# Kernel optimization log

Hardware: AMD Instinct MI355X
Metric: run time of the kernel (lower is better)

## Reference

```python
import jax, jax.numpy as jnp
import numpy as np

B, N, C, H = 4, 2048, 384, 6
D = C // H                       # head_dim = 64
HID = 4 * C                      # mlp hidden = 1536
SCALE = D ** -0.5
EPS = 1e-5                       # torch nn.LayerNorm default


def setup_inputs() -> dict:
    key = jax.random.key(0)
    ks = jax.random.split(key, 8)
    s = 0.02
    return {
        "x": jax.random.normal(ks[0], (B, N, C), jnp.float32),
        "ln1_g": jnp.ones((C,), jnp.float32),
        "ln1_b": jnp.zeros((C,), jnp.float32),
        "w_qkv": jax.random.normal(ks[1], (3 * C, C), jnp.float32) * s,
        "w_proj": jax.random.normal(ks[2], (C, C), jnp.float32) * s,
        "b_proj": jnp.zeros((C,), jnp.float32),
        "ln2_g": jnp.ones((C,), jnp.float32),
        "ln2_b": jnp.zeros((C,), jnp.float32),
        "w_fc1": jax.random.normal(ks[3], (HID, C), jnp.float32) * s,
        "b_fc1": jnp.zeros((HID,), jnp.float32),
        "w_fc2": jax.random.normal(ks[4], (C, HID), jnp.float32) * s,
        "b_fc2": jnp.zeros((C,), jnp.float32),
    }


def _layernorm(x, g, b):
    mu = jnp.mean(x, axis=-1, keepdims=True)
    var = jnp.mean(jnp.square(x - mu), axis=-1, keepdims=True)
    return (x - mu) * jax.lax.rsqrt(var + EPS) * g + b


def _bf16_round(x):
    # emulate the .bfloat16() cast after each residual (precision truncation)
    return x.astype(jnp.bfloat16).astype(jnp.float32)


def reference(x, ln1_g, ln1_b, w_qkv, w_proj, b_proj,
              ln2_g, ln2_b, w_fc1, b_fc1, w_fc2, b_fc2):
    # ---- attention branch (quant=False => HMQ ops are pass-through) ----
    h = _layernorm(x, ln1_g, ln1_b)                       # [B,N,C]
    qkv = jnp.einsum('bnc,oc->bno', h, w_qkv)             # [B,N,3C]
    qkv = qkv.reshape(B, N, 3, H, D).transpose(2, 0, 3, 1, 4)  # [3,B,H,N,D]
    q, k, v = qkv[0], qkv[1], qkv[2]
    attn = jnp.einsum('bhnd,bhmd->bhnm', q, k) * SCALE    # [B,H,N,N]
    attn = jax.nn.softmax(attn, axis=-1)
    o = jnp.einsum('bhnm,bhmd->bhnd', attn, v)            # [B,H,N,D]
    o = o.transpose(0, 2, 1, 3).reshape(B, N, C)
    o = jnp.einsum('bnc,oc->bno', o, w_proj) + b_proj
    x = _bf16_round(x + o)

    # ---- MLP branch ----
    h = _layernorm(x, ln2_g, ln2_b)
    h = jnp.einsum('bnc,hc->bnh', h, w_fc1) + b_fc1       # [B,N,HID]
    h = jax.nn.gelu(h, approximate=False)
    h = jnp.einsum('bnh,ch->bnc', h, w_fc2) + b_fc2       # [B,N,C]
    x = _bf16_round(x + h)
    return x
```

## Files before the change

### kernel.cpp

```cpp
#include <hip/hip_runtime.h>
#include <cstdint>
#include <cstddef>

#define DI __device__ __forceinline__

typedef __attribute__((ext_vector_type(8))) short short8;
typedef __attribute__((ext_vector_type(4))) float f32x4;
typedef unsigned int u32;
typedef unsigned short u16;

DI u16 rne_bf16(float f) {
  union { float f; u32 u; } v; v.f = f;
  u32 b = v.u;
  return (u16)((b + 0x7fffu + ((b >> 16) & 1u)) >> 16);
}
DI float bf2f(u16 h) {
  union { u32 u; float f; } v; v.u = ((u32)h) << 16;
  return v.f;
}

DI void gl2lds16(const void* g, void* l) {
  __builtin_amdgcn_global_load_lds(
      (const __attribute__((address_space(1))) u32*)g,
      (__attribute__((address_space(3))) u32*)l, 16, 0, 0);
}

DI void bar() {
  asm volatile("" ::: "memory");
  __builtin_amdgcn_s_barrier();
  asm volatile("" ::: "memory");
}

template<int ROWS>
DI void stage_swz(const u16* src, int ld, char* ldsb, int tid) {
  int wbase = tid & ~63;
  #pragma unroll
  for (int c = 0; c < (ROWS * 8) / 256; ++c) {
    int g = c * 256 + tid;
    int row = g >> 3;
    int sgr = (g & 7) ^ (row & 7);
    gl2lds16(src + row * ld + sgr * 8, ldsb + (size_t)(c * 256 + wbase) * 16);
  }
}

DI short8 lds_frag(const char* base, int row, int k0) {
  return *(const short8*)(base + row * 128 + ((k0 * 2) ^ ((row & 7) << 4)));
}

DI f32x4 mfma16(short8 a, short8 b, f32x4 c) {
  return __builtin_amdgcn_mfma_f32_16x16x32_bf16(a, b, c, 0, 0, 0);
}

__global__ __launch_bounds__(256) void cvt_w(
    const float* __restrict__ a, const float* __restrict__ b,
    const float* __restrict__ c, const float* __restrict__ d,
    u16* __restrict__ oa, u16* __restrict__ ob, u16* __restrict__ oc,
    u16* __restrict__ od) {
  int i = blockIdx.x * 256 + threadIdx.x;
  if (i < 442368) oa[i] = rne_bf16(a[i]);
  else if (i < 589824) ob[i - 442368] = rne_bf16(b[i - 442368]);
  else if (i < 1179648) oc[i - 589824] = rne_bf16(c[i - 589824]);
  else if (i < 1769472) od[i - 1179648] = rne_bf16(d[i - 1179648]);
}

template<int INBF>
__global__ __launch_bounds__(256) void ln_k(
    const void* __restrict__ xin, const float* __restrict__ gam,
    const float* __restrict__ bet, u16* __restrict__ out) {
  int row = blockIdx.x * 4 + (threadIdx.x >> 6);
  int lane = threadIdx.x & 63;
  float v[6];
  if (INBF) {
    const u16* x = (const u16*)xin + (size_t)row * 384 + lane * 6;
    #pragma unroll
    for (int j = 0; j < 6; ++j) v[j] = bf2f(x[j]);
  } else {
    const float* x = (const float*)xin + (size_t)row * 384 + lane * 6;
    #pragma unroll
    for (int j = 0; j < 6; ++j) v[j] = x[j];
  }
  float s = 0.f;
  #pragma unroll
  for (int j = 0; j < 6; ++j) s += v[j];
  #pragma unroll
  for (int d = 1; d < 64; d <<= 1) s += __shfl_xor(s, d);
  float mu = s * (1.f / 384.f);
  float q = 0.f;
  #pragma unroll
  for (int j = 0; j < 6; ++j) { float t = v[j] - mu; q += t * t; }
  #pragma unroll
  for (int d = 1; d < 64; d <<= 1) q += __shfl_xor(q, d);
  float rstd = rsqrtf(q * (1.f / 384.f) + 1e-5f);
  #pragma unroll
  for (int j = 0; j < 6; ++j) {
    int c = lane * 6 + j;
    out[(size_t)row * 384 + c] = rne_bf16((v[j] - mu) * rstd * gam[c] + bet[c]);
  }
}

struct EpiP {
  const float* bias;
  const float* residf;
  const u16* residb;
  u16* outb;
  float* outf;
  u16* q; u16* k; u16* v;
};

template<int EPI, int MT>
__global__ __launch_bounds__(256) void gemm_bt(
    const u16* __restrict__ A, const u16* __restrict__ W, int K, EpiP p) {
  constexpr int ABUF = MT * 128;
  constexpr int NC = (MT == 128) ? 4 : 2;
  __shared__ char lds[2 * (ABUF + 16384)];
  int tid = threadIdx.x, lane = tid & 63, wid = tid >> 6;
  int wr = (MT == 128) ? (wid >> 1) * 64 : 0;
  int wcb = (MT == 128) ? (wid & 1) * 64 : wid * 32;
  int fr = lane & 15, k8 = lane >> 4;
  int bm = blockIdx.x, bn = blockIdx.y;
  const u16* Ab = A + (size_t)bm * MT * K;
  const u16* Wb = W + (size_t)bn * 128 * K;

  stage_swz<MT>(Ab, K, lds, tid);
  stage_swz<128>(Wb, K, lds + ABUF, tid);

  f32x4 zz = {0.f, 0.f, 0.f, 0.f};
  f32x4 acc[4][NC];
  #pragma unroll
  for (int mr = 0; mr < 4; ++mr)
    #pragma unroll
    for (int nc = 0; nc < NC; ++nc) acc[mr][nc] = zz;

  asm volatile("s_waitcnt vmcnt(0)" ::: "memory");
  __syncthreads();

  int KT = K >> 6;
  for (int t = 0; t < KT; ++t) {
    char* base = lds + (size_t)(t & 1) * (ABUF + 16384);
    if (t + 1 < KT) {
      char* nb = lds + (size_t)((t + 1) & 1) * (ABUF + 16384);
      stage_swz<MT>(Ab + (t + 1) * 64, K, nb, tid);
      stage_swz<128>(Wb + (t + 1) * 64, K, nb + ABUF, tid);
    }
    #pragma unroll
    for (int ks = 0; ks < 2; ++ks) {
      int k0 = ks * 32 + k8 * 8;
      short8 av[4], bv[NC];
      #pragma unroll
      for (int mr = 0; mr < 4; ++mr) av[mr] = lds_frag(base, wr + mr * 16 + fr, k0);
      #pragma unroll
      for (int nc = 0; nc < NC; ++nc) bv[nc] = lds_frag(base + ABUF, wcb + nc * 16 + fr, k0);
      #pragma unroll
      for (int mr = 0; mr < 4; ++mr)
        #pragma unroll
        for (int nc = 0; nc < NC; ++nc)
          acc[mr][nc] = mfma16(av[mr], bv[nc], acc[mr][nc]);
    }
    asm volatile("s_waitcnt vmcnt(0)" ::: "memory");
    __syncthreads();
  }

  #pragma unroll
  for (int mr = 0; mr < 4; ++mr)
    #pragma unroll
    for (int nc = 0; nc < NC; ++nc)
      #pragma unroll
      for (int r = 0; r < 4; ++r) {
        int m = bm * MT + wr + mr * 16 + k8 * 4 + r;
        int o = bn * 128 + wcb + nc * 16 + fr;
        float val = acc[mr][nc][r];
        if constexpr (EPI == 0) {
          int tq = o / 384;
          int rem = o - tq * 384;
          int hh = rem >> 6, d = rem & 63;
          int b = m >> 11, n = m & 2047;
          u16 bvs = rne_bf16(val);
          size_t qk = (((size_t)(b * 6 + hh)) * 2048 + n) * 64 + d;
          if (tq == 0) p.q[qk] = bvs;
          else if (tq == 1) p.k[qk] = bvs;
          else p.v[qk] = bvs;
        } else if constexpr (EPI == 1) {
          size_t idx = (size_t)m * 384 + o;
          float r2 = p.residf[idx] + val + p.bias[o];
          p.outb[idx] = rne_bf16(r2);
        } else if constexpr (EPI == 2) {
          size_t idx = (size_t)m * 1536 + o;
          float z = val + p.bias[o];
          float gl = 0.5f * z * (1.f + erff(z * 0.70710678118654752f));
          p.outb[idx] = rne_bf16(gl);
        } else {
          size_t idx = (size_t)m * 384 + o;
          float r2 = bf2f(p.residb[idx]) + val + p.bias[o];
          p.outf[idx] = bf2f(rne_bf16(r2));
        }
      }
}

__global__ __launch_bounds__(256) void vtr_k(
    const u16* __restrict__ v, u16* __restrict__ vt) {
  __shared__ u16 t[64 * 72];
  int tid = threadIdx.x;
  int n0 = blockIdx.x * 64, bh = blockIdx.y;
  const u16* src = v + ((size_t)bh * 2048 + n0) * 64;
  #pragma unroll
  for (int it = 0; it < 2; ++it) {
    int row = it * 32 + (tid >> 3), c8 = tid & 7;
    *(short8*)&t[row * 72 + c8 * 8] = *(const short8*)(src + row * 64 + c8 * 8);
  }
  __syncthreads();
  int d = tid & 63, c = tid >> 6;
  u16 o[16];
  #pragma unroll
  for (int j = 0; j < 16; ++j) o[j] = t[(c * 16 + j) * 72 + d];
  u16* dst = vt + ((size_t)bh * 64 + d) * 2048 + n0 + c * 16;
  *(short8*)dst = *(short8*)&o[0];
  *(short8*)(dst + 8) = *(short8*)&o[8];
}

__global__ __launch_bounds__(256) void attn_k(
    const u16* __restrict__ Qg, const u16* __restrict__ Kg,
    const u16* __restrict__ Vg, float* __restrict__ Op, float* __restrict__ lp) {
  __shared__ char lds[65536];
  int tid = threadIdx.x, lane = tid & 63, wid = tid >> 6;
  int fr = lane & 15, k8 = lane >> 4;
  int qt = blockIdx.x, bh = blockIdx.y, z = blockIdx.z;
  const u16* Qb = Qg + (size_t)bh * 2048 * 64;
  const u16* Kb = Kg + ((size_t)bh * 2048 + z * 1024) * 64;
  const u16* Vb = Vg + (size_t)bh * 64 * 2048 + z * 1024;
  int qr0 = qt * 128 + wid * 32;

  short8 qf[2][2];
  #pragma unroll
  for (int mr = 0; mr < 2; ++mr)
    #pragma unroll
    for (int ks = 0; ks < 2; ++ks)
      qf[mr][ks] = *(const short8*)(Qb + (size_t)(qr0 + mr * 16 + fr) * 64 + ks * 32 + k8 * 8);

  f32x4 zz = {0.f, 0.f, 0.f, 0.f};
  f32x4 oacc[2][4];
  float lrun[2][4];
  #pragma unroll
  for (int mr = 0; mr < 2; ++mr) {
    #pragma unroll
    for (int nc = 0; nc < 4; ++nc) oacc[mr][nc] = zz;
    #pragma unroll
    for (int r = 0; r < 4; ++r) lrun[mr][r] = 0.f;
  }
  char* P = lds + 49152 + wid * 4096;

  #define STAGE(t)                                                            \
    stage_swz<64>(Kb + (size_t)(t) * 64 * 64, 64, lds + ((t) % 3) * 8192, tid); \
    stage_swz<64>(Vb + (t) * 64, 2048, lds + 24576 + ((t) % 3) * 8192, tid);

  STAGE(0);
  STAGE(1);
  asm volatile("s_waitcnt vmcnt(4)" ::: "memory");
  bar();

  for (int t = 0; t < 16; ++t) {
    if (t + 2 < 16) { STAGE(t + 2); }
    char* kbase = lds + (t % 3) * 8192;
    char* vbase = lds + 24576 + (t % 3) * 8192;
    f32x4 s[2][4];
    #pragma unroll
    for (int mr = 0; mr < 2; ++mr)
      #pragma unroll
      for (int nc = 0; nc < 4; ++nc) s[mr][nc] = zz;
    #pragma unroll
    for (int ks = 0; ks < 2; ++ks) {
      int k0 = ks * 32 + k8 * 8;
      short8 kf[4];
      #pragma unroll
      for (int nc = 0; nc < 4; ++nc) kf[nc] = lds_frag(kbase, nc * 16 + fr, k0);
      __builtin_amdgcn_s_setprio(1);
      #pragma unroll
      for (int mr = 0; mr < 2; ++mr)
        #pragma unroll
        for (int nc = 0; nc < 4; ++nc)
          s[mr][nc] = mfma16(qf[mr][ks], kf[nc], s[mr][nc]);
      __builtin_amdgcn_s_setprio(0);
    }
    #pragma unroll
    for (int mr = 0; mr < 2; ++mr)
      #pragma unroll
      for (int nc = 0; nc < 4; ++nc)
        #pragma unroll
        for (int r = 0; r < 4; ++r) {
          float pv = exp2f(s[mr][nc][r] * 0.18033688011112042f);
          lrun[mr][r] += pv;
          int row7 = (k8 * 4 + r) & 7;
          *(u16*)(P + (mr * 16 + k8 * 4 + r) * 128 +
                  (((nc * 16 + fr) * 2) ^ (row7 << 4))) = rne_bf16(pv);
        }
    #pragma unroll
    for (int ks = 0; ks < 2; ++ks) {
      int k0 = ks * 32 + k8 * 8;
      short8 pa[2], vf[4];
      #pragma unroll
      for (int mr = 0; mr < 2; ++mr)
        pa[mr] = *(const short8*)(P + (mr * 16 + fr) * 128 +
                                  ((k0 * 2) ^ ((fr & 7) << 4)));
      #pragma unroll
      for (int nc = 0; nc < 4; ++nc) vf[nc] = lds_frag(vbase, nc * 16 + fr, k0);
      __builtin_amdgcn_s_setprio(1);
      #pragma unroll
      for (int mr = 0; mr < 2; ++mr)
        #pragma unroll
        for (int nc = 0; nc < 4; ++nc)
          oacc[mr][nc] = mfma16(pa[mr], vf[nc], oacc[mr][nc]);
      __builtin_amdgcn_s_setprio(0);
    }
    if (t <= 13) { asm volatile("s_waitcnt vmcnt(4)" ::: "memory"); }
    else if (t == 14) { asm volatile("s_waitcnt vmcnt(0)" ::: "memory"); }
    if (t < 15) bar();
  }
  #undef STAGE

  #pragma unroll
  for (int mr = 0; mr < 2; ++mr)
    #pragma unroll
    for (int r = 0; r < 4; ++r) {
      float t2 = lrun[mr][r];
      #pragma unroll
      for (int dd = 1; dd < 16; dd <<= 1) t2 += __shfl_xor(t2, dd);
      lrun[mr][r] = t2;
    }
  size_t rowb = (size_t)z * 49152 + (size_t)bh * 2048;
  #pragma unroll
  for (int mr = 0; mr < 2; ++mr)
    #pragma unroll
    for (int nc = 0; nc < 4; ++nc)
      #pragma unroll
      for (int r = 0; r < 4; ++r) {
        int qrow = qr0 + mr * 16 + k8 * 4 + r;
        Op[(rowb + qrow) * 64 + nc * 16 + fr] = oacc[mr][nc][r];
      }
  if (fr == 0)
    #pragma unroll
    for (int mr = 0; mr < 2; ++mr)
      #pragma unroll
      for (int r = 0; r < 4; ++r)
        lp[rowb + qr0 + mr * 16 + k8 * 4 + r] = lrun[mr][r];
}

__global__ __launch_bounds__(256) void attn_merge(
    const float* __restrict__ Op, const float* __restrict__ lp,
    u16* __restrict__ ao) {
  int row = blockIdx.x * 4 + (threadIdx.x >> 6);
  int d = threadIdx.x & 63;
  float l = lp[row] + lp[49152 + row];
  float v = (Op[(size_t)row * 64 + d] + Op[(size_t)(49152 + row) * 64 + d]) / l;
  int bh = row >> 11, n = row & 2047;
  int b = bh / 6, hh = bh - b * 6;
  ao[((size_t)(b * 2048 + n)) * 384 + hh * 64 + d] = rne_bf16(v);
}

extern "C" void kernel_launch(void* const* d_in, const int* in_sizes, int n_in,
                              void* d_out, int out_size, void* d_ws, size_t ws_size,
                              hipStream_t stream) {
  const float* x     = (const float*)d_in[0];
  const float* ln1g  = (const float*)d_in[1];
  const float* ln1b  = (const float*)d_in[2];
  const float* wqkv  = (const float*)d_in[3];
  const float* wproj = (const float*)d_in[4];
  const float* bproj = (const float*)d_in[5];
  const float* ln2g  = (const float*)d_in[6];
  const float* ln2b  = (const float*)d_in[7];
  const float* wfc1  = (const float*)d_in[8];
  const float* bfc1  = (const float*)d_in[9];
  const float* wfc2  = (const float*)d_in[10];
  const float* bfc2  = (const float*)d_in[11];
  float* out = (float*)d_out;

  char* w = (char*)d_ws;
  u16* h1     = (u16*)w; w += 6291456;
  u16* x2     = (u16*)w; w += 6291456;
  u16* h2     = (u16*)w; w += 6291456;
  u16* qb     = (u16*)w; w += 6291456;
  u16* kb     = (u16*)w; w += 6291456;
  u16* vtb    = (u16*)w; w += 6291456;
  u16* ao     = (u16*)w; w += 6291456;
  u16* act    = (u16*)w; w += 25165824;
  u16* wqkvb  = (u16*)w; w += 884736;
  u16* wprojb = (u16*)w; w += 294912;
  u16* wfc1b  = (u16*)w; w += 1179648;
  u16* wfc2b  = (u16*)w; w += 1179648;

  u16* v_nat   = h2;
  float* Opart = (float*)act;
  float* lpart = (float*)h2;

  cvt_w<<<6912, 256, 0, stream>>>(wqkv, wproj, wfc1, wfc2, wqkvb, wprojb, wfc1b, wfc2b);
  ln_k<0><<<2048, 256, 0, stream>>>(x, ln1g, ln1b, h1);
  {
    EpiP p{}; p.q = qb; p.k = kb; p.v = v_nat;
    gemm_bt<0, 64><<<dim3(128, 9), 256, 0, stream>>>(h1, wqkvb, 384, p);
  }
  vtr_k<<<dim3(32, 24), 256, 0, stream>>>(v_nat, vtb);
  attn_k<<<dim3(16, 24, 2), 256, 0, stream>>>(qb, kb, vtb, Opart, lpart);
  attn_merge<<<12288, 256, 0, stream>>>(Opart, lpart, ao);
  {
    EpiP p{}; p.bias = bproj; p.residf = x; p.outb = x2;
    gemm_bt<1, 64><<<dim3(128, 3), 256, 0, stream>>>(ao, wprojb, 384, p);
  }
  ln_k<1><<<2048, 256, 0, stream>>>(x2, ln2g, ln2b, h2);
  {
    EpiP p{}; p.bias = bfc1; p.outb = act;
    gemm_bt<2, 128><<<dim3(64, 12), 256, 0, stream>>>(h2, wfc1b, 384, p);
  }
  {
    EpiP p{}; p.bias = bfc2; p.residb = x2; p.outf = out;
    gemm_bt<3, 64><<<dim3(128, 3), 256, 0, stream>>>(act, wfc2b, 1536, p);
  }
}
```

Baseline: 247.5 us.

## Restructure attention to 8 waves x16 rows, fold scale into Q, swizzle GEMM grids

The attention kernel now runs 512 threads with 8 waves, each handling 16 query rows, which shrinks per-wave registers. It uses double buffering in place of triple buffering with less LDS, and a padded per-wave P tile written via packed bf16 conversion. The softmax scale is folded into Q in the QKV GEMM epilogue, removing a multiply per score. GEMMs switch to a 1D grid with an XCD-aware block remap and raise MFMA priority. The trade-off is reduced prefetch depth, a full vmcnt(0) wait every iteration, and Q rounded to bf16 after scaling rather than before.

```diff
diff --git a/kernel.cpp b/kernel.cpp
--- a/kernel.cpp
+++ b/kernel.cpp
@@ -18,6 +18,11 @@
   union { u32 u; float f; } v; v.u = ((u32)h) << 16;
   return v.f;
 }
+DI u32 cvtpk_bf16(float a, float b) {
+  u32 r;
+  asm("v_cvt_pk_bf16_f32 %0, %1, %2" : "=v"(r) : "v"(a), "v"(b));
+  return r;
+}
 
 DI void gl2lds16(const void* g, void* l) {
   __builtin_amdgcn_global_load_lds(
@@ -31,15 +36,15 @@
   asm volatile("" ::: "memory");
 }
 
-template<int ROWS>
+template<int ROWS, int NT>
 DI void stage_swz(const u16* src, int ld, char* ldsb, int tid) {
   int wbase = tid & ~63;
   #pragma unroll
-  for (int c = 0; c < (ROWS * 8) / 256; ++c) {
-    int g = c * 256 + tid;
+  for (int c = 0; c < (ROWS * 8) / NT; ++c) {
+    int g = c * NT + tid;
     int row = g >> 3;
     int sgr = (g & 7) ^ (row & 7);
-    gl2lds16(src + row * ld + sgr * 8, ldsb + (size_t)(c * 256 + wbase) * 16);
+    gl2lds16(src + row * ld + sgr * 8, ldsb + (size_t)(c * NT + wbase) * 16);
   }
 }
 
@@ -107,9 +112,12 @@
   u16* q; u16* k; u16* v;
 };
 
+#define QSCALE 0.18033688011112042f
+
 template<int EPI, int MT>
 __global__ __launch_bounds__(256) void gemm_bt(
-    const u16* __restrict__ A, const u16* __restrict__ W, int K, EpiP p) {
+    const u16* __restrict__ A, const u16* __restrict__ W, int K, int bnN,
+    EpiP p) {
   constexpr int ABUF = MT * 128;
   constexpr int NC = (MT == 128) ? 4 : 2;
   __shared__ char lds[2 * (ABUF + 16384)];
@@ -117,12 +125,15 @@
   int wr = (MT == 128) ? (wid >> 1) * 64 : 0;
   int wcb = (MT == 128) ? (wid & 1) * 64 : wid * 32;
   int fr = lane & 15, k8 = lane >> 4;
-  int bm = blockIdx.x, bn = blockIdx.y;
+  int orig = blockIdx.x;
+  int cpx = (int)gridDim.x >> 3;
+  int wg = (orig & 7) * cpx + (orig >> 3);
+  int bm = wg / bnN, bn = wg - bm * bnN;
   const u16* Ab = A + (size_t)bm * MT * K;
   const u16* Wb = W + (size_t)bn * 128 * K;
 
-  stage_swz<MT>(Ab, K, lds, tid);
-  stage_swz<128>(Wb, K, lds + ABUF, tid);
+  stage_swz<MT, 256>(Ab, K, lds, tid);
+  stage_swz<128, 256>(Wb, K, lds + ABUF, tid);
 
   f32x4 zz = {0.f, 0.f, 0.f, 0.f};
   f32x4 acc[4][NC];
@@ -139,8 +150,8 @@
     char* base = lds + (size_t)(t & 1) * (ABUF + 16384);
     if (t + 1 < KT) {
       char* nb = lds + (size_t)((t + 1) & 1) * (ABUF + 16384);
-      stage_swz<MT>(Ab + (t + 1) * 64, K, nb, tid);
-      stage_swz<128>(Wb + (t + 1) * 64, K, nb + ABUF, tid);
+      stage_swz<MT, 256>(Ab + (t + 1) * 64, K, nb, tid);
+      stage_swz<128, 256>(Wb + (t + 1) * 64, K, nb + ABUF, tid);
     }
     #pragma unroll
     for (int ks = 0; ks < 2; ++ks) {
@@ -150,11 +161,13 @@
       for (int mr = 0; mr < 4; ++mr) av[mr] = lds_frag(base, wr + mr * 16 + fr, k0);
       #pragma unroll
       for (int nc = 0; nc < NC; ++nc) bv[nc] = lds_frag(base + ABUF, wcb + nc * 16 + fr, k0);
+      __builtin_amdgcn_s_setprio(1);
       #pragma unroll
       for (int mr = 0; mr < 4; ++mr)
         #pragma unroll
         for (int nc = 0; nc < NC; ++nc)
           acc[mr][nc] = mfma16(av[mr], bv[nc], acc[mr][nc]);
+      __builtin_amdgcn_s_setprio(0);
     }
     asm volatile("s_waitcnt vmcnt(0)" ::: "memory");
     __syncthreads();
@@ -174,7 +187,8 @@
           int rem = o - tq * 384;
           int hh = rem >> 6, d = rem & 63;
           int b = m >> 11, n = m & 2047;
-          u16 bvs = rne_bf16(val);
+          float sv = (tq == 0) ? val * QSCALE : val;
+          u16 bvs = rne_bf16(sv);
           size_t qk = (((size_t)(b * 6 + hh)) * 2048 + n) * 64 + d;
           if (tq == 0) p.q[qk] = bvs;
           else if (tq == 1) p.k[qk] = bvs;
@@ -217,55 +231,49 @@
   *(short8*)(dst + 8) = *(short8*)&o[8];
 }
 
-__global__ __launch_bounds__(256) void attn_k(
+__global__ __launch_bounds__(512, 6) void attn_k(
     const u16* __restrict__ Qg, const u16* __restrict__ Kg,
     const u16* __restrict__ Vg, float* __restrict__ Op, float* __restrict__ lp) {
-  __shared__ char lds[65536];
+  __shared__ char lds[51712];
   int tid = threadIdx.x, lane = tid & 63, wid = tid >> 6;
   int fr = lane & 15, k8 = lane >> 4;
   int qt = blockIdx.x, bh = blockIdx.y, z = blockIdx.z;
   const u16* Qb = Qg + (size_t)bh * 2048 * 64;
   const u16* Kb = Kg + ((size_t)bh * 2048 + z * 1024) * 64;
   const u16* Vb = Vg + (size_t)bh * 64 * 2048 + z * 1024;
-  int qr0 = qt * 128 + wid * 32;
-
-  short8 qf[2][2];
-  #pragma unroll
-  for (int mr = 0; mr < 2; ++mr)
-    #pragma unroll
-    for (int ks = 0; ks < 2; ++ks)
-      qf[mr][ks] = *(const short8*)(Qb + (size_t)(qr0 + mr * 16 + fr) * 64 + ks * 32 + k8 * 8);
+  int qr0 = qt * 128 + wid * 16;
+
+  short8 qf[2];
+  #pragma unroll
+  for (int ks = 0; ks < 2; ++ks)
+    qf[ks] = *(const short8*)(Qb + (size_t)(qr0 + fr) * 64 + ks * 32 + k8 * 8);
 
   f32x4 zz = {0.f, 0.f, 0.f, 0.f};
-  f32x4 oacc[2][4];
-  float lrun[2][4];
-  #pragma unroll
-  for (int mr = 0; mr < 2; ++mr) {
-    #pragma unroll
-    for (int nc = 0; nc < 4; ++nc) oacc[mr][nc] = zz;
-    #pragma unroll
-    for (int r = 0; r < 4; ++r) lrun[mr][r] = 0.f;
-  }
-  char* P = lds + 49152 + wid * 4096;
-
-  #define STAGE(t)                                                            \
-    stage_swz<64>(Kb + (size_t)(t) * 64 * 64, 64, lds + ((t) % 3) * 8192, tid); \
-    stage_swz<64>(Vb + (t) * 64, 2048, lds + 24576 + ((t) % 3) * 8192, tid);
+  f32x4 oacc[4];
+  float lrun[4];
+  #pragma unroll
+  for (int nc = 0; nc < 4; ++nc) oacc[nc] = zz;
+  #pragma unroll
+  for (int r = 0; r < 4; ++r) lrun[r] = 0.f;
+  char* P = lds + 32768 + wid * 2368;
+  char* Pw = P + (k8 * 4) * 148 + fr * 2;
+  char* Pr = P + fr * 148;
+
+  #define STAGE(t)                                                             \
+    stage_swz<64, 512>(Kb + (size_t)(t) * 4096, 64, lds + ((t) & 1) * 8192, tid); \
+    stage_swz<64, 512>(Vb + (t) * 64, 2048, lds + 16384 + ((t) & 1) * 8192, tid);
 
   STAGE(0);
-  STAGE(1);
-  asm volatile("s_waitcnt vmcnt(4)" ::: "memory");
+  asm volatile("s_waitcnt vmcnt(0)" ::: "memory");
   bar();
 
   for (int t = 0; t < 16; ++t) {
-    if (t + 2 < 16) { STAGE(t + 2); }
-    char* kbase = lds + (t % 3) * 8192;
-    char* vbase = lds + 24576 + (t % 3) * 8192;
-    f32x4 s[2][4];
-    #pragma unroll
-    for (int mr = 0; mr < 2; ++mr)
-      #pragma unroll
-      for (int nc = 0; nc < 4; ++nc) s[mr][nc] = zz;
+    if (t + 1 < 16) { STAGE(t + 1); }
+    char* kbase = lds + (t & 1) * 8192;
+    char* vbase = lds + 16384 + (t & 1) * 8192;
+    f32x4 s[4];
+    #pragma unroll
+    for (int nc = 0; nc < 4; ++nc) s[nc] = zz;
     #pragma unroll
     for (int ks = 0; ks < 2; ++ks) {
       int k0 = ks * 32 + k8 * 8;
@@ -274,73 +282,57 @@
       for (int nc = 0; nc < 4; ++nc) kf[nc] = lds_frag(kbase, nc * 16 + fr, k0);
       __builtin_amdgcn_s_setprio(1);
       #pragma unroll
-      for (int mr = 0; mr < 2; ++mr)
-        #pragma unroll
-        for (int nc = 0; nc < 4; ++nc)
-          s[mr][nc] = mfma16(qf[mr][ks], kf[nc], s[mr][nc]);
+      for (int nc = 0; nc < 4; ++nc) s[nc] = mfma16(qf[ks], kf[nc], s[nc]);
       __builtin_amdgcn_s_setprio(0);
     }
     #pragma unroll
-    for (int mr = 0; mr < 2; ++mr)
-      #pragma unroll
-      for (int nc = 0; nc < 4; ++nc)
-        #pragma unroll
-        for (int r = 0; r < 4; ++r) {
-          float pv = exp2f(s[mr][nc][r] * 0.18033688011112042f);
-          lrun[mr][r] += pv;
-          int row7 = (k8 * 4 + r) & 7;
-          *(u16*)(P + (mr * 16 + k8 * 4 + r) * 128 +
-                  (((nc * 16 + fr) * 2) ^ (row7 << 4))) = rne_bf16(pv);
-        }
+    for (int nc = 0; nc < 4; ++nc)
+      #pragma unroll
+      for (int rp = 0; rp < 2; ++rp) {
+        float p0 = exp2f(s[nc][2 * rp]);
+        float p1 = exp2f(s[nc][2 * rp + 1]);
+        lrun[2 * rp] += p0;
+        lrun[2 * rp + 1] += p1;
+        u32 w = cvtpk_bf16(p0, p1);
+        *(u16*)(Pw + (2 * rp) * 148 + nc * 32) = (u16)w;
+        *(u16*)(Pw + (2 * rp + 1) * 148 + nc * 32) = (u16)(w >> 16);
+      }
     #pragma unroll
     for (int ks = 0; ks < 2; ++ks) {
       int k0 = ks * 32 + k8 * 8;
-      short8 pa[2], vf[4];
-      #pragma unroll
-      for (int mr = 0; mr < 2; ++mr)
-        pa[mr] = *(const short8*)(P + (mr * 16 + fr) * 128 +
-                                  ((k0 * 2) ^ ((fr & 7) << 4)));
+      short8 pa = *(const short8*)(Pr + k0 * 2);
+      short8 vf[4];
       #pragma unroll
       for (int nc = 0; nc < 4; ++nc) vf[nc] = lds_frag(vbase, nc * 16 + fr, k0);
       __builtin_amdgcn_s_setprio(1);
       #pragma unroll
-      for (int mr = 0; mr < 2; ++mr)
-        #pragma unroll
-        for (int nc = 0; nc < 4; ++nc)
-          oacc[mr][nc] = mfma16(pa[mr], vf[nc], oacc[mr][nc]);
+      for (int nc = 0; nc < 4; ++nc) oacc[nc] = mfma16(pa, vf[nc], oacc[nc]);
       __builtin_amdgcn_s_setprio(0);
     }
-    if (t <= 13) { asm volatile("s_waitcnt vmcnt(4)" ::: "memory"); }
-    else if (t == 14) { asm volatile("s_waitcnt vmcnt(0)" ::: "memory"); }
+    asm volatile("s_waitcnt vmcnt(0)" ::: "memory");
     if (t < 15) bar();
   }
   #undef STAGE
 
   #pragma unroll
-  for (int mr = 0; mr < 2; ++mr)
+  for (int r = 0; r < 4; ++r) {
+    float t2 = lrun[r];
+    #pragma unroll
+    for (int dd = 1; dd < 16; dd <<= 1) t2 += __shfl_xor(t2, dd);
+    lrun[r] = t2;
+  }
+  size_t rowb = (size_t)z * 49152 + (size_t)bh * 2048;
+  #pragma unroll
+  for (int nc = 0; nc < 4; ++nc)
     #pragma unroll
     for (int r = 0; r < 4; ++r) {
-      float t2 = lrun[mr][r];
-      #pragma unroll
-      for (int dd = 1; dd < 16; dd <<= 1) t2 += __shfl_xor(t2, dd);
-      lrun[mr][r] = t2;
+      int qrow = qr0 + k8 * 4 + r;
+      Op[(rowb + qrow) * 64 + nc * 16 + fr] = oacc[nc][r];
     }
-  size_t rowb = (size_t)z * 49152 + (size_t)bh * 2048;
-  #pragma unroll
-  for (int mr = 0; mr < 2; ++mr)
-    #pragma unroll
-    for (int nc = 0; nc < 4; ++nc)
-      #pragma unroll
-      for (int r = 0; r < 4; ++r) {
-        int qrow = qr0 + mr * 16 + k8 * 4 + r;
-        Op[(rowb + qrow) * 64 + nc * 16 + fr] = oacc[mr][nc][r];
-      }
   if (fr == 0)
     #pragma unroll
-    for (int mr = 0; mr < 2; ++mr)
-      #pragma unroll
-      for (int r = 0; r < 4; ++r)
-        lp[rowb + qr0 + mr * 16 + k8 * 4 + r] = lrun[mr][r];
+    for (int r = 0; r < 4; ++r)
+      lp[rowb + qr0 + k8 * 4 + r] = lrun[r];
 }
 
 __global__ __launch_bounds__(256) void attn_merge(
@@ -394,22 +386,22 @@
   ln_k<0><<<2048, 256, 0, stream>>>(x, ln1g, ln1b, h1);
   {
     EpiP p{}; p.q = qb; p.k = kb; p.v = v_nat;
-    gemm_bt<0, 64><<<dim3(128, 9), 256, 0, stream>>>(h1, wqkvb, 384, p);
+    gemm_bt<0, 64><<<1152, 256, 0, stream>>>(h1, wqkvb, 384, 9, p);
   }
   vtr_k<<<dim3(32, 24), 256, 0, stream>>>(v_nat, vtb);
-  attn_k<<<dim3(16, 24, 2), 256, 0, stream>>>(qb, kb, vtb, Opart, lpart);
+  attn_k<<<dim3(16, 24, 2), 512, 0, stream>>>(qb, kb, vtb, Opart, lpart);
   attn_merge<<<12288, 256, 0, stream>>>(Opart, lpart, ao);
   {
     EpiP p{}; p.bias = bproj; p.residf = x; p.outb = x2;
-    gemm_bt<1, 64><<<dim3(128, 3), 256, 0, stream>>>(ao, wprojb, 384, p);
+    gemm_bt<1, 64><<<384, 256, 0, stream>>>(ao, wprojb, 384, 3, p);
   }
   ln_k<1><<<2048, 256, 0, stream>>>(x2, ln2g, ln2b, h2);
   {
     EpiP p{}; p.bias = bfc1; p.outb = act;
-    gemm_bt<2, 128><<<dim3(64, 12), 256, 0, stream>>>(h2, wfc1b, 384, p);
+    gemm_bt<2, 128><<<768, 256, 0, stream>>>(h2, wfc1b, 384, 12, p);
   }
   {
     EpiP p{}; p.bias = bfc2; p.residb = x2; p.outf = out;
-    gemm_bt<3, 64><<<dim3(128, 3), 256, 0, stream>>>(act, wfc2b, 1536, p);
-  }
-}
+    gemm_bt<3, 64><<<384, 256, 0, stream>>>(act, wfc2b, 1536, 3, p);
+  }
+}
```

Measured after the change: 247.4 us. About the same (-0.0%).
